# Kernel optimization log

Hardware: AMD Instinct MI355X
Metric: run time of the kernel (lower is better)

The kernel has to match this reference:

```python
import jax, jax.numpy as jnp
import numpy as np

BATCH, SEQ, HIDDEN = 4, 4096, 2880
NUM_EXPERTS, TOP_K = 128, 4


def setup_inputs() -> dict:
    key = jax.random.key(0)
    k1, k2, k3, k4, k5 = jax.random.split(key, 5)
    hidden_states = jax.random.normal(k1, (BATCH, SEQ, HIDDEN), dtype=jnp.float32)
    modality_mask = jax.random.randint(k2, (BATCH, SEQ), 0, 2) == 1  # True = vision token
    weight = jax.random.normal(k3, (NUM_EXPERTS, HIDDEN), dtype=jnp.float32) * 0.02
    bias = jax.random.normal(k4, (NUM_EXPERTS,), dtype=jnp.float32) * 0.02
    vision_bias = jax.random.normal(k5, (NUM_EXPERTS,), dtype=jnp.float32) * 0.02
    return {
        "hidden_states": hidden_states,
        "modality_mask": modality_mask,
        "weight": weight,
        "bias": bias,
        "vision_bias": vision_bias,
    }


def reference(hidden_states, modality_mask, weight, bias, vision_bias):
    # Flatten tokens: (num_tokens, hidden_dim)
    x = hidden_states.reshape(-1, hidden_states.shape[-1])
    mm = modality_mask.reshape(-1)  # (num_tokens,) bool

    # router_logits = x @ W^T + b, then add vision bias only for vision tokens
    logits = jnp.einsum("td,ed->te", x, weight) + bias  # (T, E)
    logits = logits + jnp.where(mm[:, None], vision_bias.astype(logits.dtype), 0.0)

    # top-k over experts, softmax over the selected k logits
    top_vals, top_idx = jax.lax.top_k(logits, TOP_K)      # (T, k)
    top_probs = jax.nn.softmax(top_vals, axis=-1)

    # scatter normalized probs back into a dense (T, E) score matrix
    T = logits.shape[0]
    rows = jnp.arange(T)[:, None]
    router_scores = jnp.zeros_like(logits).at[rows, top_idx].set(top_probs)
    return router_scores, top_idx
```

## Files before the change

### kernel.cpp

```cpp
#include <hip/hip_runtime.h>

constexpr int T_TOK = 16384;
constexpr int NEXP  = 128;
constexpr int HID   = 2880;
constexpr int TOPK  = 4;

constexpr int KSPLIT = 8;
constexpr int KCH    = HID / 32;
constexpr int BM     = 128;
constexpr int BK     = 32;
constexpr int WELEMS = NEXP * HID;

typedef __attribute__((ext_vector_type(8))) short bf16x8;
typedef __attribute__((ext_vector_type(4))) float f32x4;

__device__ inline void split3(float f, unsigned& hb, unsigned& mb, unsigned& lb) {
    unsigned u = __float_as_uint(f);
    unsigned rne = u + 0x7FFFu + ((u >> 16) & 1u);
    hb = rne & 0xFFFF0000u;
    float r = f - __uint_as_float(hb);
    mb = __float_as_uint(r) & 0xFFFF0000u;
    lb = __float_as_uint(r - __uint_as_float(mb));
}

__global__ __launch_bounds__(256)
void w_split_kernel(const float* __restrict__ w, unsigned short* __restrict__ wh,
                    unsigned short* __restrict__ wm, unsigned short* __restrict__ wl) {
    int i = blockIdx.x * 256 + threadIdx.x;
    if (i < WELEMS) {
        unsigned hb, mb, lb;
        split3(w[i], hb, mb, lb);
        wh[i] = (unsigned short)(hb >> 16);
        wm[i] = (unsigned short)(mb >> 16);
        wl[i] = (unsigned short)(lb >> 16);
    }
}

__global__ __launch_bounds__(256, 2)
void gemm_mfma(const float* __restrict__ x,
               const unsigned short* __restrict__ wh,
               const unsigned short* __restrict__ wm,
               const unsigned short* __restrict__ wl,
               float* __restrict__ part) {
    __shared__ unsigned short bs[2][3 * NEXP * BK];

    const int tid  = threadIdx.x;
    const int wv   = tid >> 6;
    const int lane = tid & 63;
    const int lm   = lane & 15;
    const int lq   = lane >> 4;

    const int tile  = blockIdx.x / KSPLIT;
    const int split = blockIdx.x % KSPLIT;
    const int kcb   = (KCH * split) / KSPLIT;
    const int nit   = (KCH * (split + 1)) / KSPLIT - kcb;

    f32x4 acc[2][8];
#pragma unroll
    for (int i = 0; i < 2; ++i)
#pragma unroll
        for (int j = 0; j < 8; ++j) acc[i][j] = (f32x4){0.f, 0.f, 0.f, 0.f};

    const float* xb = x + (size_t)tile * BM * HID;

    auto stage = [&](int it, int buf) {
        const int k0 = (kcb + it) * 32;
#pragma unroll
        for (int r = 0; r < 6; ++r) {
            const int c  = (r * 4 + wv) * 64 + lane;
            const int cc = c & 511;
            const int e  = cc >> 2;
            const int kq = (cc & 3) << 3;
            const unsigned short* plane = (r < 2) ? wh : (r < 4) ? wm : wl;
            const unsigned short* src = plane + (size_t)e * HID + k0 + kq;
            __builtin_amdgcn_global_load_lds(
                (const __attribute__((address_space(1))) void*)src,
                (__attribute__((address_space(3))) void*)&bs[buf][c * 8], 16, 0, 0);
        }
    };
    auto loadx = [&](int it, float4 xr[2][2]) {
        const int k0 = (kcb + it) * 32;
#pragma unroll
        for (int i = 0; i < 2; ++i) {
            const float* ap = xb + (size_t)(wv * 32 + i * 16 + lm) * HID + k0 + lq * 8;
            xr[i][0] = *reinterpret_cast<const float4*>(ap);
            xr[i][1] = *reinterpret_cast<const float4*>(ap + 4);
        }
    };

    float4 xr[2][2];
    stage(0, 0);
    loadx(0, xr);

    for (int it = 0; it < nit; ++it) {
        const int cur = it & 1;
        __syncthreads();
        if (it + 1 < nit) stage(it + 1, cur ^ 1);

        unsigned ah[2][4], am[2][4], al[2][4];
#pragma unroll
        for (int i = 0; i < 2; ++i) {
            float fv[8] = {xr[i][0].x, xr[i][0].y, xr[i][0].z, xr[i][0].w,
                           xr[i][1].x, xr[i][1].y, xr[i][1].z, xr[i][1].w};
            unsigned hb[8], mb[8], lb[8];
#pragma unroll
            for (int e2 = 0; e2 < 8; ++e2) split3(fv[e2], hb[e2], mb[e2], lb[e2]);
#pragma unroll
            for (int p = 0; p < 4; ++p) {
                ah[i][p] = __builtin_amdgcn_perm(hb[2*p+1], hb[2*p], 0x07060302u);
                am[i][p] = __builtin_amdgcn_perm(mb[2*p+1], mb[2*p], 0x07060302u);
                al[i][p] = __builtin_amdgcn_perm(lb[2*p+1], lb[2*p], 0x07060302u);
            }
        }
        if (it + 1 < nit) loadx(it + 1, xr);

#pragma unroll
        for (int j = 0; j < 8; ++j) {
            const int boff = (j * 16 + lm) * BK + lq * 8;
            bf16x8 Bh = *reinterpret_cast<const bf16x8*>(&bs[cur][boff]);
            bf16x8 Bm = *reinterpret_cast<const bf16x8*>(&bs[cur][NEXP * BK + boff]);
            bf16x8 Bl = *reinterpret_cast<const bf16x8*>(&bs[cur][2 * NEXP * BK + boff]);
#pragma unroll
            for (int i = 0; i < 2; ++i) {
                union { unsigned u[4]; bf16x8 v; } Ah, Am, Al;
#pragma unroll
                for (int p = 0; p < 4; ++p) {
                    Ah.u[p] = ah[i][p]; Am.u[p] = am[i][p]; Al.u[p] = al[i][p];
                }
                acc[i][j] = __builtin_amdgcn_mfma_f32_16x16x32_bf16(Ah.v, Bh, acc[i][j], 0, 0, 0);
                acc[i][j] = __builtin_amdgcn_mfma_f32_16x16x32_bf16(Ah.v, Bm, acc[i][j], 0, 0, 0);
                acc[i][j] = __builtin_amdgcn_mfma_f32_16x16x32_bf16(Am.v, Bh, acc[i][j], 0, 0, 0);
                acc[i][j] = __builtin_amdgcn_mfma_f32_16x16x32_bf16(Am.v, Bm, acc[i][j], 0, 0, 0);
                acc[i][j] = __builtin_amdgcn_mfma_f32_16x16x32_bf16(Ah.v, Bl, acc[i][j], 0, 0, 0);
                acc[i][j] = __builtin_amdgcn_mfma_f32_16x16x32_bf16(Al.v, Bh, acc[i][j], 0, 0, 0);
            }
        }
    }

#pragma unroll
    for (int i = 0; i < 2; ++i) {
        const int trow = tile * BM + wv * 32 + i * 16 + lq * 4;
#pragma unroll
        for (int j = 0; j < 8; ++j) {
            const int e = j * 16 + lm;
            float* p = part + ((size_t)split * T_TOK + trow) * NEXP + e;
#pragma unroll
            for (int r = 0; r < 4; ++r) p[(size_t)r * NEXP] = acc[i][j][r];
        }
    }
}

__global__ __launch_bounds__(256)
void topk_scatter(const float* __restrict__ part, const int* __restrict__ mm,
                  const float* __restrict__ bias, const float* __restrict__ vbias,
                  float* __restrict__ out) {
    const int lane = threadIdx.x & 63;
    const int wid  = threadIdx.x >> 6;
    const int t    = blockIdx.x * 4 + wid;

    const int e0 = lane, e1 = 64 + lane;
    float v0 = bias[e0];
    float v1 = bias[e1];
    if (mm[t] != 0) { v0 += vbias[e0]; v1 += vbias[e1]; }
#pragma unroll
    for (int s = 0; s < KSPLIT; ++s) {
        const float* p = part + ((size_t)s * T_TOK + t) * NEXP;
        v0 += p[e0];
        v1 += p[e1];
    }

    float lv0 = v0, lv1 = v1;
    float tv[TOPK];
    int   ti[TOPK];
#pragma unroll
    for (int k = 0; k < TOPK; ++k) {
        float bv; int bi;
        if (lv0 >= lv1) { bv = lv0; bi = e0; }
        else            { bv = lv1; bi = e1; }
#pragma unroll
        for (int off = 32; off >= 1; off >>= 1) {
            float ov = __shfl_xor(bv, off, 64);
            int   oi = __shfl_xor(bi, off, 64);
            if (ov > bv || (ov == bv && oi < bi)) { bv = ov; bi = oi; }
        }
        tv[k] = bv;
        ti[k] = bi;
        if (bi == e0) lv0 = -__builtin_inff();
        if (bi == e1) lv1 = -__builtin_inff();
    }

    const float m = tv[0];
    float ex[TOPK], s = 0.f;
#pragma unroll
    for (int k = 0; k < TOPK; ++k) { ex[k] = expf(tv[k] - m); s += ex[k]; }
    const float inv = 1.0f / s;

    float s0 = 0.f, s1 = 0.f;
#pragma unroll
    for (int k = 0; k < TOPK; ++k) {
        const float p = ex[k] * inv;
        if (ti[k] == e0) s0 = p;
        if (ti[k] == e1) s1 = p;
    }
    out[(size_t)t * NEXP + e0] = s0;
    out[(size_t)t * NEXP + e1] = s1;
    if (lane < TOPK)
        out[(size_t)T_TOK * NEXP + (size_t)t * TOPK + lane] = (float)ti[lane];
}

extern "C" void kernel_launch(void* const* d_in, const int* in_sizes, int n_in,
                              void* d_out, int out_size, void* d_ws, size_t ws_size,
                              hipStream_t stream) {
    const float* x     = (const float*)d_in[0];
    const int*   mm    = (const int*)d_in[1];
    const float* w     = (const float*)d_in[2];
    const float* bias  = (const float*)d_in[3];
    const float* vbias = (const float*)d_in[4];
    float* out  = (float*)d_out;

    float* part = (float*)d_ws;
    const size_t part_bytes = (size_t)KSPLIT * T_TOK * NEXP * sizeof(float);
    unsigned short* whp = (unsigned short*)((char*)d_ws + part_bytes);
    unsigned short* wmp = whp + WELEMS;
    unsigned short* wlp = wmp + WELEMS;

    hipLaunchKernelGGL(w_split_kernel, dim3((WELEMS + 255) / 256), dim3(256), 0,
                       stream, w, whp, wmp, wlp);
    hipLaunchKernelGGL(gemm_mfma, dim3((T_TOK / BM) * KSPLIT), dim3(256), 0, stream,
                       x, whp, wmp, wlp, part);
    hipLaunchKernelGGL(topk_scatter, dim3(T_TOK / 4), dim3(256), 0, stream,
                       part, mm, bias, vbias, out);
}
```

Baseline: 310.8 us.

## Reduce K-split to 6, raise GEMM occupancy, precompute addresses, vectorize top-k loads

Lowers the K-split factor from 8 to 6 so each GEMM block runs a fixed 15-iteration loop, which also shrinks the partial-sum buffer the top-k kernel reads. Launch bounds now request 3 blocks per SM, and the global and LDS source addresses are computed once before the loop instead of every iteration. The top-k kernel gives each lane two adjacent experts, so its loads and stores become float2. The trade-offs are fewer GEMM blocks, more register pressure from the occupancy hint and the hoisted pointers, and a tie-break order that changes with the new expert-to-lane mapping.

```diff
diff --git a/kernel.cpp b/kernel.cpp
--- a/kernel.cpp
+++ b/kernel.cpp
@@ -5,8 +5,9 @@
 constexpr int HID   = 2880;
 constexpr int TOPK  = 4;
 
-constexpr int KSPLIT = 8;
+constexpr int KSPLIT = 6;
 constexpr int KCH    = HID / 32;
+constexpr int NIT    = KCH / KSPLIT;
 constexpr int BM     = 128;
 constexpr int BK     = 32;
 constexpr int WELEMS = NEXP * HID;
@@ -36,7 +37,7 @@
     }
 }
 
-__global__ __launch_bounds__(256, 2)
+__global__ __launch_bounds__(256, 3)
 void gemm_mfma(const float* __restrict__ x,
                const unsigned short* __restrict__ wh,
                const unsigned short* __restrict__ wm,
@@ -52,8 +53,7 @@
 
     const int tile  = blockIdx.x / KSPLIT;
     const int split = blockIdx.x % KSPLIT;
-    const int kcb   = (KCH * split) / KSPLIT;
-    const int nit   = (KCH * (split + 1)) / KSPLIT - kcb;
+    const int kcb   = NIT * split;
 
     f32x4 acc[2][8];
 #pragma unroll
@@ -63,26 +63,35 @@
 
     const float* xb = x + (size_t)tile * BM * HID;
 
+    const unsigned short* srcp[6];
+    int cidx[6];
+#pragma unroll
+    for (int r = 0; r < 6; ++r) {
+        const int c  = (r * 4 + wv) * 64 + lane;
+        const int cc = c & 511;
+        const int e  = cc >> 2;
+        const int kq = (cc & 3) << 3;
+        const unsigned short* plane = (r < 2) ? wh : (r < 4) ? wm : wl;
+        srcp[r] = plane + (size_t)e * HID + kcb * 32 + kq;
+        cidx[r] = c;
+    }
+    const float* xp[2];
+#pragma unroll
+    for (int i = 0; i < 2; ++i)
+        xp[i] = xb + (size_t)(wv * 32 + i * 16 + lm) * HID + kcb * 32 + lq * 8;
+
     auto stage = [&](int it, int buf) {
-        const int k0 = (kcb + it) * 32;
 #pragma unroll
         for (int r = 0; r < 6; ++r) {
-            const int c  = (r * 4 + wv) * 64 + lane;
-            const int cc = c & 511;
-            const int e  = cc >> 2;
-            const int kq = (cc & 3) << 3;
-            const unsigned short* plane = (r < 2) ? wh : (r < 4) ? wm : wl;
-            const unsigned short* src = plane + (size_t)e * HID + k0 + kq;
             __builtin_amdgcn_global_load_lds(
-                (const __attribute__((address_space(1))) void*)src,
-                (__attribute__((address_space(3))) void*)&bs[buf][c * 8], 16, 0, 0);
+                (const __attribute__((address_space(1))) void*)(srcp[r] + it * 32),
+                (__attribute__((address_space(3))) void*)&bs[buf][cidx[r] * 8], 16, 0, 0);
         }
     };
     auto loadx = [&](int it, float4 xr[2][2]) {
-        const int k0 = (kcb + it) * 32;
 #pragma unroll
         for (int i = 0; i < 2; ++i) {
-            const float* ap = xb + (size_t)(wv * 32 + i * 16 + lm) * HID + k0 + lq * 8;
+            const float* ap = xp[i] + it * 32;
             xr[i][0] = *reinterpret_cast<const float4*>(ap);
             xr[i][1] = *reinterpret_cast<const float4*>(ap + 4);
         }
@@ -92,10 +101,11 @@
     stage(0, 0);
     loadx(0, xr);
 
-    for (int it = 0; it < nit; ++it) {
+#pragma unroll 1
+    for (int it = 0; it < NIT; ++it) {
         const int cur = it & 1;
         __syncthreads();
-        if (it + 1 < nit) stage(it + 1, cur ^ 1);
+        if (it + 1 < NIT) stage(it + 1, cur ^ 1);
 
         unsigned ah[2][4], am[2][4], al[2][4];
 #pragma unroll
@@ -112,7 +122,7 @@
                 al[i][p] = __builtin_amdgcn_perm(lb[2*p+1], lb[2*p], 0x07060302u);
             }
         }
-        if (it + 1 < nit) loadx(it + 1, xr);
+        if (it + 1 < NIT) loadx(it + 1, xr);
 
 #pragma unroll
         for (int j = 0; j < 8; ++j) {
@@ -158,15 +168,19 @@
     const int wid  = threadIdx.x >> 6;
     const int t    = blockIdx.x * 4 + wid;
 
-    const int e0 = lane, e1 = 64 + lane;
-    float v0 = bias[e0];
-    float v1 = bias[e1];
-    if (mm[t] != 0) { v0 += vbias[e0]; v1 += vbias[e1]; }
+    const int e0 = 2 * lane, e1 = 2 * lane + 1;
+    float2 b2 = *reinterpret_cast<const float2*>(&bias[e0]);
+    float v0 = b2.x, v1 = b2.y;
+    if (mm[t] != 0) {
+        float2 vb2 = *reinterpret_cast<const float2*>(&vbias[e0]);
+        v0 += vb2.x; v1 += vb2.y;
+    }
 #pragma unroll
     for (int s = 0; s < KSPLIT; ++s) {
         const float* p = part + ((size_t)s * T_TOK + t) * NEXP;
-        v0 += p[e0];
-        v1 += p[e1];
+        float2 pv = *reinterpret_cast<const float2*>(&p[e0]);
+        v0 += pv.x;
+        v1 += pv.y;
     }
 
     float lv0 = v0, lv1 = v1;
@@ -202,8 +216,7 @@
         if (ti[k] == e0) s0 = p;
         if (ti[k] == e1) s1 = p;
     }
-    out[(size_t)t * NEXP + e0] = s0;
-    out[(size_t)t * NEXP + e1] = s1;
+    *reinterpret_cast<float2*>(&out[(size_t)t * NEXP + e0]) = make_float2(s0, s1);
     if (lane < TOPK)
         out[(size_t)T_TOK * NEXP + (size_t)t * TOPK + lane] = (float)ti[lane];
 }
```

New measurement: 302.5 us. 1.03x faster.
